# Kernel optimization log

Hardware: AMD Instinct MI355X
Metric: run time of the kernel (lower is better)

## Reference

```python
import jax, jax.numpy as jnp
import numpy as np

B, C, D = 2, 2048, 1024   # batch, seq_len, hidden_size
I = 2048                  # intermediate_size (GLU hidden)
E, K = 8, 2               # n_experts, top_k
CF = 1.25                 # capacity factor


def setup_inputs() -> dict:
    key = jax.random.key(0)
    k1, k2, k3, k4 = jax.random.split(key, 4)
    scale = 0.02
    return {
        "hidden_states": jax.random.normal(k1, (B, C, D), jnp.float32),
        "Wg": jax.random.normal(k2, (E, D), jnp.float32) * scale,      # router gate weight [E, d]
        "W1": jax.random.normal(k3, (E, D, 2 * I), jnp.float32) * scale,  # expert in-proj
        "W2": jax.random.normal(k4, (E, I, D), jnp.float32) * scale,      # expert out-proj
    }


def reference(hidden_states, Wg, W1, W2):
    Bx, Cx, d = hidden_states.shape
    N = Bx * Cx
    cap = int(N * K * CF / E)  # exp_capacity (static)
    x = hidden_states.reshape(N, d)

    # --- router (eval mode: no noise) ---
    logits = x @ Wg.T                          # [N, E]
    top_v, top_i = jax.lax.top_k(logits, K)    # [N, K]
    gates = jax.nn.softmax(top_v, axis=-1)     # [N, K]

    # --- greedy capacity-limited assignment (token-major, then k), vectorized ---
    flat_e = top_i.reshape(N * K)              # expert id per (token, k) slot, in loop order
    gates_f = gates.reshape(N * K)
    tok = jnp.repeat(jnp.arange(N), K)         # token id per slot
    onehot = jax.nn.one_hot(flat_e, E, dtype=jnp.int32)
    pos = jnp.cumsum(onehot, axis=0) - 1       # running count per expert
    pos_f = jnp.take_along_axis(pos, flat_e[:, None], axis=1)[:, 0]
    keep = pos_f < cap                         # slots beyond capacity are dropped
    pos_safe = jnp.where(keep, pos_f, cap)     # out-of-range -> dropped by mode='drop'

    # --- dispatch: exp_batches[e, pos] = x[token] ---
    exp_batches = jnp.zeros((E, cap, d), x.dtype).at[flat_e, pos_safe].set(x[tok], mode='drop')

    # --- per-expert GLU MLP (batched over experts) ---
    h = jnp.einsum('ecd,edf->ecf', exp_batches, W1)       # [E, cap, 2I]
    inp, gate = jnp.split(h, 2, axis=-1)
    h = jax.nn.gelu(inp, approximate=False) * gate        # exact gelu, matches torch
    exp_out = jnp.einsum('eci,eid->ecd', h, W2)           # [E, cap, d]

    # --- combine: equals exp_mask.view(N,-1) @ exp_out.view(-1,d) ---
    gathered = exp_out[flat_e, jnp.minimum(pos_safe, cap - 1)]  # [N*K, d]
    contrib = jnp.where(keep, gates_f, 0.0)[:, None] * gathered
    out = jax.ops.segment_sum(contrib, tok, num_segments=N)    # [N, d]
    return out.reshape(Bx, Cx, d)
```

## Files before the change

### kernel.cpp

```cpp
#include <hip/hip_runtime.h>
#include <hip/hip_bf16.h>
#include <math.h>

#define N_TOK 4096
#define DIM   1024
#define NEXP  8
#define IDIM  2048
#define TWOI  4096
#define CAP   1280

#define W1_BLOCKS (64 * 16 * NEXP)
#define W2_BLOCKS (16 * 32 * NEXP)
#define ROUTER_BLOCKS (N_TOK / 4)

#define G1X 32
#define G1Y 10
#define G1_TRANS_Z ((W2_BLOCKS + G1X * G1Y - 1) / (G1X * G1Y))

using short8  = __attribute__((ext_vector_type(8))) short;
using floatx4 = __attribute__((ext_vector_type(4))) float;

__device__ __forceinline__ unsigned short f2b(float f) {
  __hip_bfloat16 h = __float2bfloat16(f);
  return *reinterpret_cast<unsigned short*>(&h);
}

__device__ __forceinline__ void async16(const unsigned short* g, unsigned short* l) {
  __builtin_amdgcn_global_load_lds(
      (const __attribute__((address_space(1))) unsigned int*)g,
      (__attribute__((address_space(3))) unsigned int*)l,
      16, 0, 0);
}

__global__ __launch_bounds__(256) void prologue_kernel(const float* __restrict__ W1,
                                                       unsigned short* __restrict__ w1t,
                                                       const float* __restrict__ x,
                                                       const float* __restrict__ Wg,
                                                       unsigned short* __restrict__ xb,
                                                       float* __restrict__ out,
                                                       int* __restrict__ top_i,
                                                       float* __restrict__ gates) {
  __shared__ __align__(16) float smem_f[NEXP * DIM];
  int bid = blockIdx.x;
  int tid = threadIdx.x;

  if (bid < W1_BLOCKS) {
    float (*tile)[65] = reinterpret_cast<float (*)[65]>(smem_f);
    int e = bid >> 10;
    int t = bid & 1023;
    const int R = DIM, C = TWOI;
    int r0 = (t & 15) * 64;
    int c0 = (t >> 4) * 64;
    const float* s = W1 + (size_t)e * R * C;
    unsigned short* d = w1t + (size_t)e * R * C;
    int tr = tid >> 4, tc = (tid & 15) * 4;
#pragma unroll
    for (int i = 0; i < 4; i++) {
      float4 v = *reinterpret_cast<const float4*>(&s[(size_t)(r0 + tr + i * 16) * C + c0 + tc]);
      tile[tr + i * 16][tc]     = v.x;
      tile[tr + i * 16][tc + 1] = v.y;
      tile[tr + i * 16][tc + 2] = v.z;
      tile[tr + i * 16][tc + 3] = v.w;
    }
    __syncthreads();
#pragma unroll
    for (int j = 0; j < 4; j++) {
      int c = (tid >> 4) + j * 16;
      int r4 = (tid & 15) * 4;
      ushort4 o;
      o.x = f2b(tile[r4][c]);
      o.y = f2b(tile[r4 + 1][c]);
      o.z = f2b(tile[r4 + 2][c]);
      o.w = f2b(tile[r4 + 3][c]);
      *reinterpret_cast<ushort4*>(&d[(size_t)(c0 + c) * R + r0 + r4]) = o;
    }
  } else {
    int rb = bid - W1_BLOCKS;
    float* wg = smem_f;
    for (int i = tid * 4; i < NEXP * DIM; i += 256 * 4) {
      *reinterpret_cast<float4*>(wg + i) = *reinterpret_cast<const float4*>(Wg + i);
    }
    __syncthreads();
    int wave = tid >> 6, lane = tid & 63;
    int t = rb * 4 + wave;
    const float* xr = x + (size_t)t * DIM;
    unsigned short* xbr = xb + (size_t)t * DIM;
    float* outr = out + (size_t)t * DIM;
    double acc[NEXP];
#pragma unroll
    for (int e = 0; e < NEXP; e++) acc[e] = 0.0;
    for (int i = lane; i < DIM; i += 64) {
      float xf = xr[i];
      xbr[i] = f2b(xf);
      outr[i] = 0.0f;
      double xv = (double)xf;
#pragma unroll
      for (int e = 0; e < NEXP; e++) acc[e] += xv * (double)wg[e * DIM + i];
    }
#pragma unroll
    for (int e = 0; e < NEXP; e++) {
#pragma unroll
      for (int m = 1; m < 64; m <<= 1) acc[e] += __shfl_xor(acc[e], m, 64);
    }
    if (lane == 0) {
      int i0 = 0; double v0 = acc[0];
      for (int e = 1; e < NEXP; e++) { if (acc[e] > v0) { v0 = acc[e]; i0 = e; } }
      int i1 = -1; double v1 = -1e300;
      for (int e = 0; e < NEXP; e++) { if (e != i0 && acc[e] > v1) { v1 = acc[e]; i1 = e; } }
      double e1 = exp(v1 - v0);
      float g0 = (float)(1.0 / (1.0 + e1));
      float g1 = (float)(e1 / (1.0 + e1));
      top_i[t * 2] = i0; top_i[t * 2 + 1] = i1;
      gates[t * 2] = g0; gates[t * 2 + 1] = g1;
    }
  }
}

__global__ __launch_bounds__(1024) void scan_kernel(const int* __restrict__ top_i,
                                                    const float* __restrict__ gates,
                                                    int* __restrict__ rowtok,
                                                    float* __restrict__ rowgate,
                                                    int* __restrict__ cnt) {
  __shared__ int hist[NEXP][1024];
  int t = threadIdx.x;
  int s0 = t * 8;
  int eloc[8];
  int c[NEXP];
#pragma unroll
  for (int e = 0; e < NEXP; e++) c[e] = 0;
#pragma unroll
  for (int j = 0; j < 8; j++) { int e = top_i[s0 + j]; eloc[j] = e; c[e]++; }
#pragma unroll
  for (int e = 0; e < NEXP; e++) hist[e][t] = c[e];
  __syncthreads();
  for (int step = 1; step < 1024; step <<= 1) {
    int tmp[NEXP];
#pragma unroll
    for (int e = 0; e < NEXP; e++) tmp[e] = (t >= step) ? hist[e][t - step] : 0;
    __syncthreads();
#pragma unroll
    for (int e = 0; e < NEXP; e++) hist[e][t] += tmp[e];
    __syncthreads();
  }
  int base[NEXP];
#pragma unroll
  for (int e = 0; e < NEXP; e++) base[e] = hist[e][t] - c[e];
  if (t < NEXP) {
    int tot = hist[t][1023];
    cnt[t] = tot < CAP ? tot : CAP;
  }
#pragma unroll
  for (int j = 0; j < 8; j++) {
    int s = s0 + j;
    int e = eloc[j];
    int pos = base[e]++;
    if (pos < CAP) {
      rowtok[e * CAP + pos] = s >> 1;
      rowgate[e * CAP + pos] = gates[s];
    }
  }
}

__global__ __launch_bounds__(256, 4) void gemm1_kernel(const unsigned short* __restrict__ xb,
                                                       const unsigned short* __restrict__ w1t,
                                                       const int* __restrict__ rowtok,
                                                       const int* __restrict__ cnt,
                                                       unsigned short* __restrict__ H,
                                                       const float* __restrict__ W2,
                                                       unsigned short* __restrict__ w2t) {
  __shared__ __align__(16) unsigned char smem[64 * 65 * 4];
  int tid  = threadIdx.x;
  int z = blockIdx.z;

  if (z >= NEXP) {
    int id = (z - NEXP) * (G1X * G1Y) + blockIdx.y * G1X + blockIdx.x;
    if (id >= W2_BLOCKS) return;
    float (*tile)[65] = reinterpret_cast<float (*)[65]>(smem);
    int e = id >> 9;
    int t = id & 511;
    const int R = IDIM, C = DIM;
    int r0 = (t & 31) * 64;
    int c0 = (t >> 5) * 64;
    const float* s = W2 + (size_t)e * R * C;
    unsigned short* d = w2t + (size_t)e * R * C;
    int tr = tid >> 4, tc = (tid & 15) * 4;
#pragma unroll
    for (int i = 0; i < 4; i++) {
      float4 v = *reinterpret_cast<const float4*>(&s[(size_t)(r0 + tr + i * 16) * C + c0 + tc]);
      tile[tr + i * 16][tc]     = v.x;
      tile[tr + i * 16][tc + 1] = v.y;
      tile[tr + i * 16][tc + 2] = v.z;
      tile[tr + i * 16][tc + 3] = v.w;
    }
    __syncthreads();
#pragma unroll
    for (int j = 0; j < 4; j++) {
      int c = (tid >> 4) + j * 16;
      int r4 = (tid & 15) * 4;
      ushort4 o;
      o.x = f2b(tile[r4][c]);
      o.y = f2b(tile[r4 + 1][c]);
      o.z = f2b(tile[r4 + 2][c]);
      o.w = f2b(tile[r4 + 3][c]);
      *reinterpret_cast<ushort4*>(&d[(size_t)(c0 + c) * R + r0 + r4]) = o;
    }
    return;
  }

  int e  = z;
  int m0 = blockIdx.y * 128;
  int i0 = blockIdx.x * 64;
  int cnte = cnt[e];
  if (m0 >= cnte) return;

  unsigned short* As = reinterpret_cast<unsigned short*>(smem);
  unsigned short* Bi = reinterpret_cast<unsigned short*>(smem + 8192);
  unsigned short* Bg = reinterpret_cast<unsigned short*>(smem + 12288);

  int lane = tid & 63;
  int wave = tid >> 6;

  int srA0 = wave * 32 + (lane >> 2);
  int srA1 = srA0 + 16;
  int srB  = wave * 16 + (lane >> 2);
  int sk   = (lane & 3) * 8;

  int ma0 = m0 + srA0, ma1 = m0 + srA1;
  int tok0 = (ma0 < cnte) ? rowtok[e * CAP + ma0] : 0;
  int tok1 = (ma1 < cnte) ? rowtok[e * CAP + ma1] : 0;

  const unsigned short* w1e = w1t + (size_t)e * TWOI * DIM;
  const unsigned short* gA0 = xb + (size_t)tok0 * DIM + sk;
  const unsigned short* gA1 = xb + (size_t)tok1 * DIM + sk;
  const unsigned short* gBi = w1e + (size_t)(i0 + srB) * DIM + sk;
  const unsigned short* gBg = w1e + (size_t)(i0 + srB + IDIM) * DIM + sk;

  unsigned short* lA0 = As + (wave * 2 + 0) * 512;
  unsigned short* lA1 = As + (wave * 2 + 1) * 512;
  unsigned short* lBi = Bi + wave * 512;
  unsigned short* lBg = Bg + wave * 512;

  int lane16 = lane & 15;
  int quad   = lane >> 4;
  int wm = (wave & 1) * 64;
  int wn = (wave >> 1) * 32;

  floatx4 acc_i[4][2], acc_g[4][2];
#pragma unroll
  for (int i = 0; i < 4; i++)
#pragma unroll
    for (int j = 0; j < 2; j++) {
      acc_i[i][j] = (floatx4){0.f, 0.f, 0.f, 0.f};
      acc_g[i][j] = (floatx4){0.f, 0.f, 0.f, 0.f};
    }

  for (int k0 = 0; k0 < DIM; k0 += 32) {
    __syncthreads();
    async16(gA0 + k0, lA0);
    async16(gA1 + k0, lA1);
    async16(gBi + k0, lBi);
    async16(gBg + k0, lBg);
    __syncthreads();

    short8 a[4];
#pragma unroll
    for (int i = 0; i < 4; i++)
      a[i] = *(const short8*)&As[(wm + i * 16 + lane16) * 32 + quad * 8];
#pragma unroll
    for (int j = 0; j < 2; j++) {
      short8 bi = *(const short8*)&Bi[(wn + j * 16 + lane16) * 32 + quad * 8];
#pragma unroll
      for (int i = 0; i < 4; i++)
        acc_i[i][j] = __builtin_amdgcn_mfma_f32_16x16x32_bf16(a[i], bi, acc_i[i][j], 0, 0, 0);
      short8 bg = *(const short8*)&Bg[(wn + j * 16 + lane16) * 32 + quad * 8];
#pragma unroll
      for (int i = 0; i < 4; i++)
        acc_g[i][j] = __builtin_amdgcn_mfma_f32_16x16x32_bf16(a[i], bg, acc_g[i][j], 0, 0, 0);
    }
  }

  unsigned short* He = H + (size_t)e * CAP * IDIM;
#pragma unroll
  for (int i = 0; i < 4; i++) {
#pragma unroll
    for (int r = 0; r < 4; r++) {
      int m = m0 + wm + i * 16 + quad * 4 + r;
#pragma unroll
      for (int j = 0; j < 2; j++) {
        int n = i0 + wn + j * 16 + lane16;
        float vi = acc_i[i][j][r];
        float vg = acc_g[i][j][r];
        float h = 0.5f * vi * (1.0f + erff(vi * 0.70710678118654752f)) * vg;
        He[(size_t)m * IDIM + n] = f2b(h);
      }
    }
  }
}

__global__ __launch_bounds__(256, 3) void gemm2_kernel(const unsigned short* __restrict__ H,
                                                       const unsigned short* __restrict__ w2t,
                                                       const int* __restrict__ cnt,
                                                       const int* __restrict__ rowtok,
                                                       const float* __restrict__ rowgate,
                                                       float* __restrict__ out) {
  int e  = blockIdx.z & 7;
  int kh = blockIdx.z >> 3;
  int m0 = blockIdx.y * 128;
  int n0 = blockIdx.x * 128;
  int cnte = cnt[e];
  if (m0 >= cnte) return;

  __shared__ __align__(16) unsigned short As[128 * 32];
  __shared__ __align__(16) unsigned short Bs[128 * 32];

  int tid  = threadIdx.x;
  int lane = tid & 63;
  int wave = tid >> 6;

  int sr0 = wave * 32 + (lane >> 2);
  int sr1 = sr0 + 16;
  int sk  = (lane & 3) * 8;
  int kbase = kh * (IDIM / 2);

  const unsigned short* He  = H + (size_t)e * CAP * IDIM;
  const unsigned short* w2e = w2t + (size_t)e * DIM * IDIM;
  const unsigned short* gA0 = He + (size_t)(m0 + sr0) * IDIM + kbase + sk;
  const unsigned short* gA1 = He + (size_t)(m0 + sr1) * IDIM + kbase + sk;
  const unsigned short* gB0 = w2e + (size_t)(n0 + sr0) * IDIM + kbase + sk;
  const unsigned short* gB1 = w2e + (size_t)(n0 + sr1) * IDIM + kbase + sk;

  unsigned short* lA0 = As + (wave * 2 + 0) * 512;
  unsigned short* lA1 = As + (wave * 2 + 1) * 512;
  unsigned short* lB0 = Bs + (wave * 2 + 0) * 512;
  unsigned short* lB1 = Bs + (wave * 2 + 1) * 512;

  int lane16 = lane & 15;
  int quad   = lane >> 4;
  int wm = (wave & 1) * 64;
  int wn = (wave >> 1) * 64;

  floatx4 acc[4][4];
#pragma unroll
  for (int i = 0; i < 4; i++)
#pragma unroll
    for (int j = 0; j < 4; j++) acc[i][j] = (floatx4){0.f, 0.f, 0.f, 0.f};

  for (int k0 = 0; k0 < IDIM / 2; k0 += 32) {
    __syncthreads();
    async16(gA0 + k0, lA0);
    async16(gA1 + k0, lA1);
    async16(gB0 + k0, lB0);
    async16(gB1 + k0, lB1);
    __syncthreads();

    short8 a[4];
#pragma unroll
    for (int i = 0; i < 4; i++)
      a[i] = *(const short8*)&As[(wm + i * 16 + lane16) * 32 + quad * 8];
#pragma unroll
    for (int j = 0; j < 4; j++) {
      short8 b = *(const short8*)&Bs[(wn + j * 16 + lane16) * 32 + quad * 8];
#pragma unroll
      for (int i = 0; i < 4; i++)
        acc[i][j] = __builtin_amdgcn_mfma_f32_16x16x32_bf16(a[i], b, acc[i][j], 0, 0, 0);
    }
  }

#pragma unroll
  for (int i = 0; i < 4; i++) {
#pragma unroll
    for (int r = 0; r < 4; r++) {
      int m = m0 + wm + i * 16 + quad * 4 + r;
      if (m < cnte) {
        int tok = rowtok[e * CAP + m];
        float g = rowgate[e * CAP + m];
        float* orow = out + (size_t)tok * DIM;
#pragma unroll
        for (int j = 0; j < 4; j++) {
          int n = n0 + wn + j * 16 + lane16;
          atomicAdd(orow + n, g * acc[i][j][r]);
        }
      }
    }
  }
}

extern "C" void kernel_launch(void* const* d_in, const int* in_sizes, int n_in,
                              void* d_out, int out_size, void* d_ws, size_t ws_size,
                              hipStream_t stream) {
  const float* x  = (const float*)d_in[0];
  const float* Wg = (const float*)d_in[1];
  const float* W1 = (const float*)d_in[2];
  const float* W2 = (const float*)d_in[3];
  float* out = (float*)d_out;

  char* ws = (char*)d_ws;
  size_t off = 0;
  auto alloc = [&](size_t bytes) -> void* {
    void* p = ws + off;
    off = (off + bytes + 255) & ~(size_t)255;
    return p;
  };
  int*   top_i   = (int*)alloc((size_t)N_TOK * 2 * sizeof(int));
  float* gates   = (float*)alloc((size_t)N_TOK * 2 * sizeof(float));
  int*   rowtok  = (int*)alloc((size_t)NEXP * CAP * sizeof(int));
  float* rowgate = (float*)alloc((size_t)NEXP * CAP * sizeof(float));
  int*   cnt     = (int*)alloc((size_t)NEXP * sizeof(int));
  unsigned short* xb  = (unsigned short*)alloc((size_t)N_TOK * DIM * 2);
  unsigned short* w1t = (unsigned short*)alloc((size_t)NEXP * TWOI * DIM * 2);
  unsigned short* w2t = (unsigned short*)alloc((size_t)NEXP * DIM * IDIM * 2);
  unsigned short* Hb  = (unsigned short*)alloc((size_t)NEXP * CAP * IDIM * 2);
  if (off > ws_size) return;

  hipLaunchKernelGGL(prologue_kernel, dim3(W1_BLOCKS + ROUTER_BLOCKS), dim3(256), 0, stream,
                     W1, w1t, x, Wg, xb, out, top_i, gates);
  hipLaunchKernelGGL(scan_kernel, dim3(1), dim3(1024), 0, stream,
                     top_i, gates, rowtok, rowgate, cnt);
  hipLaunchKernelGGL(gemm1_kernel, dim3(G1X, G1Y, NEXP + G1_TRANS_Z), dim3(256), 0, stream,
                     xb, w1t, rowtok, cnt, Hb, W2, w2t);
  hipLaunchKernelGGL(gemm2_kernel, dim3(DIM / 128, CAP / 128, 16), dim3(256), 0, stream,
                     Hb, w2t, cnt, rowtok, rowgate, out);
}
```

Baseline: 471.5 us.

## Replace gemm2 atomic scatter with partial-sum buffers and a gather combine kernel

gemm2 no longer applies gates and atomically adds into the output. It now writes plain fp32 partial results for each K-half and expert into a workspace buffer. A new combine kernel gathers each token's two expert slots from both halves, applies the gates, and writes the output directly, so the prologue no longer zeroes out. This removes contended float atomics and gives deterministic accumulation, at the cost of an extra ~84MB write plus gather read and one more launch. Gemm2 launch bounds are also raised to target 4 blocks per CU.

```diff
diff --git a/kernel.cpp b/kernel.cpp
--- a/kernel.cpp
+++ b/kernel.cpp
@@ -37,7 +37,6 @@
                                                        const float* __restrict__ x,
                                                        const float* __restrict__ Wg,
                                                        unsigned short* __restrict__ xb,
-                                                       float* __restrict__ out,
                                                        int* __restrict__ top_i,
                                                        float* __restrict__ gates) {
   __shared__ __align__(16) float smem_f[NEXP * DIM];
@@ -85,14 +84,12 @@
     int t = rb * 4 + wave;
     const float* xr = x + (size_t)t * DIM;
     unsigned short* xbr = xb + (size_t)t * DIM;
-    float* outr = out + (size_t)t * DIM;
     double acc[NEXP];
 #pragma unroll
     for (int e = 0; e < NEXP; e++) acc[e] = 0.0;
     for (int i = lane; i < DIM; i += 64) {
       float xf = xr[i];
       xbr[i] = f2b(xf);
-      outr[i] = 0.0f;
       double xv = (double)xf;
 #pragma unroll
       for (int e = 0; e < NEXP; e++) acc[e] += xv * (double)wg[e * DIM + i];
@@ -119,7 +116,8 @@
 __global__ __launch_bounds__(1024) void scan_kernel(const int* __restrict__ top_i,
                                                     const float* __restrict__ gates,
                                                     int* __restrict__ rowtok,
-                                                    float* __restrict__ rowgate,
+                                                    int* __restrict__ slotpos,
+                                                    float* __restrict__ tokgate,
                                                     int* __restrict__ cnt) {
   __shared__ int hist[NEXP][1024];
   int t = threadIdx.x;
@@ -154,10 +152,10 @@
     int s = s0 + j;
     int e = eloc[j];
     int pos = base[e]++;
-    if (pos < CAP) {
-      rowtok[e * CAP + pos] = s >> 1;
-      rowgate[e * CAP + pos] = gates[s];
-    }
+    bool keep = pos < CAP;
+    slotpos[s] = keep ? pos : 0;
+    tokgate[s] = keep ? gates[s] : 0.0f;
+    if (keep) rowtok[e * CAP + pos] = s >> 1;
   }
 }
 
@@ -297,12 +295,10 @@
   }
 }
 
-__global__ __launch_bounds__(256, 3) void gemm2_kernel(const unsigned short* __restrict__ H,
+__global__ __launch_bounds__(256, 4) void gemm2_kernel(const unsigned short* __restrict__ H,
                                                        const unsigned short* __restrict__ w2t,
                                                        const int* __restrict__ cnt,
-                                                       const int* __restrict__ rowtok,
-                                                       const float* __restrict__ rowgate,
-                                                       float* __restrict__ out) {
+                                                       float* __restrict__ expoutP) {
   int e  = blockIdx.z & 7;
   int kh = blockIdx.z >> 3;
   int m0 = blockIdx.y * 128;
@@ -366,23 +362,42 @@
     }
   }
 
+  float* oute = expoutP + ((size_t)kh * NEXP + e) * CAP * DIM;
 #pragma unroll
   for (int i = 0; i < 4; i++) {
 #pragma unroll
     for (int r = 0; r < 4; r++) {
       int m = m0 + wm + i * 16 + quad * 4 + r;
-      if (m < cnte) {
-        int tok = rowtok[e * CAP + m];
-        float g = rowgate[e * CAP + m];
-        float* orow = out + (size_t)tok * DIM;
-#pragma unroll
-        for (int j = 0; j < 4; j++) {
-          int n = n0 + wn + j * 16 + lane16;
-          atomicAdd(orow + n, g * acc[i][j][r]);
-        }
+#pragma unroll
+      for (int j = 0; j < 4; j++) {
+        int n = n0 + wn + j * 16 + lane16;
+        oute[(size_t)m * DIM + n] = acc[i][j][r];
       }
     }
   }
+}
+
+__global__ __launch_bounds__(256) void combine_kernel(const int* __restrict__ top_i,
+                                                      const int* __restrict__ slotpos,
+                                                      const float* __restrict__ tokgate,
+                                                      const float* __restrict__ expoutP,
+                                                      float* __restrict__ out) {
+  int t = blockIdx.x;
+  int tid = threadIdx.x;
+  int e0 = top_i[t * 2], e1 = top_i[t * 2 + 1];
+  int p0 = slotpos[t * 2], p1 = slotpos[t * 2 + 1];
+  float g0 = tokgate[t * 2], g1 = tokgate[t * 2 + 1];
+  const float4* a0 = reinterpret_cast<const float4*>(expoutP + ((size_t)e0 * CAP + p0) * DIM);
+  const float4* a1 = reinterpret_cast<const float4*>(expoutP + ((size_t)(NEXP + e0) * CAP + p0) * DIM);
+  const float4* b0 = reinterpret_cast<const float4*>(expoutP + ((size_t)e1 * CAP + p1) * DIM);
+  const float4* b1 = reinterpret_cast<const float4*>(expoutP + ((size_t)(NEXP + e1) * CAP + p1) * DIM);
+  float4 va0 = a0[tid], va1 = a1[tid], vb0 = b0[tid], vb1 = b1[tid];
+  float4 o;
+  o.x = g0 * (va0.x + va1.x) + g1 * (vb0.x + vb1.x);
+  o.y = g0 * (va0.y + va1.y) + g1 * (vb0.y + vb1.y);
+  o.z = g0 * (va0.z + va1.z) + g1 * (vb0.z + vb1.z);
+  o.w = g0 * (va0.w + va1.w) + g1 * (vb0.w + vb1.w);
+  reinterpret_cast<float4*>(out + (size_t)t * DIM)[tid] = o;
 }
 
 extern "C" void kernel_launch(void* const* d_in, const int* in_sizes, int n_in,
@@ -404,20 +419,24 @@
   int*   top_i   = (int*)alloc((size_t)N_TOK * 2 * sizeof(int));
   float* gates   = (float*)alloc((size_t)N_TOK * 2 * sizeof(float));
   int*   rowtok  = (int*)alloc((size_t)NEXP * CAP * sizeof(int));
-  float* rowgate = (float*)alloc((size_t)NEXP * CAP * sizeof(float));
+  int*   slotpos = (int*)alloc((size_t)N_TOK * 2 * sizeof(int));
+  float* tokgate = (float*)alloc((size_t)N_TOK * 2 * sizeof(float));
   int*   cnt     = (int*)alloc((size_t)NEXP * sizeof(int));
   unsigned short* xb  = (unsigned short*)alloc((size_t)N_TOK * DIM * 2);
   unsigned short* w1t = (unsigned short*)alloc((size_t)NEXP * TWOI * DIM * 2);
   unsigned short* w2t = (unsigned short*)alloc((size_t)NEXP * DIM * IDIM * 2);
   unsigned short* Hb  = (unsigned short*)alloc((size_t)NEXP * CAP * IDIM * 2);
+  float* expoutP = (float*)alloc((size_t)2 * NEXP * CAP * DIM * sizeof(float));
   if (off > ws_size) return;
 
   hipLaunchKernelGGL(prologue_kernel, dim3(W1_BLOCKS + ROUTER_BLOCKS), dim3(256), 0, stream,
-                     W1, w1t, x, Wg, xb, out, top_i, gates);
+                     W1, w1t, x, Wg, xb, top_i, gates);
   hipLaunchKernelGGL(scan_kernel, dim3(1), dim3(1024), 0, stream,
-                     top_i, gates, rowtok, rowgate, cnt);
+                     top_i, gates, rowtok, slotpos, tokgate, cnt);
   hipLaunchKernelGGL(gemm1_kernel, dim3(G1X, G1Y, NEXP + G1_TRANS_Z), dim3(256), 0, stream,
                      xb, w1t, rowtok, cnt, Hb, W2, w2t);
   hipLaunchKernelGGL(gemm2_kernel, dim3(DIM / 128, CAP / 128, 16), dim3(256), 0, stream,
-                     Hb, w2t, cnt, rowtok, rowgate, out);
-}
+                     Hb, w2t, cnt, expoutP);
+  hipLaunchKernelGGL(combine_kernel, dim3(N_TOK), dim3(256), 0, stream,
+                     top_i, slotpos, tokgate, expoutP, out);
+}
```

New measurement: 459.1 us. 1.03x faster.

## Replace atomic combine with per-slot output buffer, drop split-K, double K-step per barrier

Applied to the files above, without the earlier changes.

The second GEMM no longer splits K across two blocks or scatters into the output with atomicAdd. Each (token, slot) row is written once into a scratch buffer, and a new combine kernel sums the two slots per token using the kept-gate mask. Both GEMMs now stage two 32-wide K chunks per barrier pair, halving synchronisations in exchange for more LDS. gemm2 occupancy is raised to 4, and the output-zeroing pass in the prologue is removed. The cost is an extra kernel launch, a 32MB scratch write and read, and fewer gemm2 blocks now that split-K is gone.

```diff
diff --git a/kernel.cpp b/kernel.cpp
--- a/kernel.cpp
+++ b/kernel.cpp
@@ -37,7 +37,6 @@
                                                        const float* __restrict__ x,
                                                        const float* __restrict__ Wg,
                                                        unsigned short* __restrict__ xb,
-                                                       float* __restrict__ out,
                                                        int* __restrict__ top_i,
                                                        float* __restrict__ gates) {
   __shared__ __align__(16) float smem_f[NEXP * DIM];
@@ -85,14 +84,12 @@
     int t = rb * 4 + wave;
     const float* xr = x + (size_t)t * DIM;
     unsigned short* xbr = xb + (size_t)t * DIM;
-    float* outr = out + (size_t)t * DIM;
     double acc[NEXP];
 #pragma unroll
     for (int e = 0; e < NEXP; e++) acc[e] = 0.0;
     for (int i = lane; i < DIM; i += 64) {
       float xf = xr[i];
       xbr[i] = f2b(xf);
-      outr[i] = 0.0f;
       double xv = (double)xf;
 #pragma unroll
       for (int e = 0; e < NEXP; e++) acc[e] += xv * (double)wg[e * DIM + i];
@@ -119,7 +116,9 @@
 __global__ __launch_bounds__(1024) void scan_kernel(const int* __restrict__ top_i,
                                                     const float* __restrict__ gates,
                                                     int* __restrict__ rowtok,
+                                                    int* __restrict__ rowslot,
                                                     float* __restrict__ rowgate,
+                                                    float* __restrict__ tokgate,
                                                     int* __restrict__ cnt) {
   __shared__ int hist[NEXP][1024];
   int t = threadIdx.x;
@@ -154,8 +153,11 @@
     int s = s0 + j;
     int e = eloc[j];
     int pos = base[e]++;
-    if (pos < CAP) {
-      rowtok[e * CAP + pos] = s >> 1;
+    bool keep = pos < CAP;
+    tokgate[s] = keep ? gates[s] : 0.0f;
+    if (keep) {
+      rowtok[e * CAP + pos]  = s >> 1;
+      rowslot[e * CAP + pos] = s & 1;
       rowgate[e * CAP + pos] = gates[s];
     }
   }
@@ -168,7 +170,7 @@
                                                        unsigned short* __restrict__ H,
                                                        const float* __restrict__ W2,
                                                        unsigned short* __restrict__ w2t) {
-  __shared__ __align__(16) unsigned char smem[64 * 65 * 4];
+  __shared__ __align__(16) unsigned char smem[32768];
   int tid  = threadIdx.x;
   int z = blockIdx.z;
 
@@ -213,9 +215,9 @@
   int cnte = cnt[e];
   if (m0 >= cnte) return;
 
-  unsigned short* As = reinterpret_cast<unsigned short*>(smem);
-  unsigned short* Bi = reinterpret_cast<unsigned short*>(smem + 8192);
-  unsigned short* Bg = reinterpret_cast<unsigned short*>(smem + 12288);
+  unsigned short* As[2] = { (unsigned short*)smem,           (unsigned short*)(smem + 8192) };
+  unsigned short* Bi[2] = { (unsigned short*)(smem + 16384), (unsigned short*)(smem + 20480) };
+  unsigned short* Bg[2] = { (unsigned short*)(smem + 24576), (unsigned short*)(smem + 28672) };
 
   int lane = tid & 63;
   int wave = tid >> 6;
@@ -235,11 +237,6 @@
   const unsigned short* gBi = w1e + (size_t)(i0 + srB) * DIM + sk;
   const unsigned short* gBg = w1e + (size_t)(i0 + srB + IDIM) * DIM + sk;
 
-  unsigned short* lA0 = As + (wave * 2 + 0) * 512;
-  unsigned short* lA1 = As + (wave * 2 + 1) * 512;
-  unsigned short* lBi = Bi + wave * 512;
-  unsigned short* lBg = Bg + wave * 512;
-
   int lane16 = lane & 15;
   int quad   = lane >> 4;
   int wm = (wave & 1) * 64;
@@ -254,28 +251,35 @@
       acc_g[i][j] = (floatx4){0.f, 0.f, 0.f, 0.f};
     }
 
-  for (int k0 = 0; k0 < DIM; k0 += 32) {
-    __syncthreads();
-    async16(gA0 + k0, lA0);
-    async16(gA1 + k0, lA1);
-    async16(gBi + k0, lBi);
-    async16(gBg + k0, lBg);
-    __syncthreads();
-
-    short8 a[4];
-#pragma unroll
-    for (int i = 0; i < 4; i++)
-      a[i] = *(const short8*)&As[(wm + i * 16 + lane16) * 32 + quad * 8];
-#pragma unroll
-    for (int j = 0; j < 2; j++) {
-      short8 bi = *(const short8*)&Bi[(wn + j * 16 + lane16) * 32 + quad * 8];
+  for (int k0 = 0; k0 < DIM; k0 += 64) {
+    __syncthreads();
+#pragma unroll
+    for (int b = 0; b < 2; b++) {
+      int kk = k0 + b * 32;
+      async16(gA0 + kk, As[b] + (wave * 2 + 0) * 512);
+      async16(gA1 + kk, As[b] + (wave * 2 + 1) * 512);
+      async16(gBi + kk, Bi[b] + wave * 512);
+      async16(gBg + kk, Bg[b] + wave * 512);
+    }
+    __syncthreads();
+
+#pragma unroll
+    for (int b = 0; b < 2; b++) {
+      short8 a[4];
 #pragma unroll
       for (int i = 0; i < 4; i++)
-        acc_i[i][j] = __builtin_amdgcn_mfma_f32_16x16x32_bf16(a[i], bi, acc_i[i][j], 0, 0, 0);
-      short8 bg = *(const short8*)&Bg[(wn + j * 16 + lane16) * 32 + quad * 8];
-#pragma unroll
-      for (int i = 0; i < 4; i++)
-        acc_g[i][j] = __builtin_amdgcn_mfma_f32_16x16x32_bf16(a[i], bg, acc_g[i][j], 0, 0, 0);
+        a[i] = *(const short8*)&As[b][(wm + i * 16 + lane16) * 32 + quad * 8];
+#pragma unroll
+      for (int j = 0; j < 2; j++) {
+        short8 bi = *(const short8*)&Bi[b][(wn + j * 16 + lane16) * 32 + quad * 8];
+#pragma unroll
+        for (int i = 0; i < 4; i++)
+          acc_i[i][j] = __builtin_amdgcn_mfma_f32_16x16x32_bf16(a[i], bi, acc_i[i][j], 0, 0, 0);
+        short8 bg = *(const short8*)&Bg[b][(wn + j * 16 + lane16) * 32 + quad * 8];
+#pragma unroll
+        for (int i = 0; i < 4; i++)
+          acc_g[i][j] = __builtin_amdgcn_mfma_f32_16x16x32_bf16(a[i], bg, acc_g[i][j], 0, 0, 0);
+      }
     }
   }
 
@@ -297,21 +301,22 @@
   }
 }
 
-__global__ __launch_bounds__(256, 3) void gemm2_kernel(const unsigned short* __restrict__ H,
+__global__ __launch_bounds__(256, 4) void gemm2_kernel(const unsigned short* __restrict__ H,
                                                        const unsigned short* __restrict__ w2t,
                                                        const int* __restrict__ cnt,
                                                        const int* __restrict__ rowtok,
+                                                       const int* __restrict__ rowslot,
                                                        const float* __restrict__ rowgate,
-                                                       float* __restrict__ out) {
-  int e  = blockIdx.z & 7;
-  int kh = blockIdx.z >> 3;
+                                                       float* __restrict__ out2) {
+  int e  = blockIdx.z;
   int m0 = blockIdx.y * 128;
   int n0 = blockIdx.x * 128;
   int cnte = cnt[e];
   if (m0 >= cnte) return;
 
-  __shared__ __align__(16) unsigned short As[128 * 32];
-  __shared__ __align__(16) unsigned short Bs[128 * 32];
+  __shared__ __align__(16) unsigned char smem[32768];
+  unsigned short* As[2] = { (unsigned short*)smem,           (unsigned short*)(smem + 8192) };
+  unsigned short* Bs[2] = { (unsigned short*)(smem + 16384), (unsigned short*)(smem + 24576) };
 
   int tid  = threadIdx.x;
   int lane = tid & 63;
@@ -320,19 +325,13 @@
   int sr0 = wave * 32 + (lane >> 2);
   int sr1 = sr0 + 16;
   int sk  = (lane & 3) * 8;
-  int kbase = kh * (IDIM / 2);
 
   const unsigned short* He  = H + (size_t)e * CAP * IDIM;
   const unsigned short* w2e = w2t + (size_t)e * DIM * IDIM;
-  const unsigned short* gA0 = He + (size_t)(m0 + sr0) * IDIM + kbase + sk;
-  const unsigned short* gA1 = He + (size_t)(m0 + sr1) * IDIM + kbase + sk;
-  const unsigned short* gB0 = w2e + (size_t)(n0 + sr0) * IDIM + kbase + sk;
-  const unsigned short* gB1 = w2e + (size_t)(n0 + sr1) * IDIM + kbase + sk;
-
-  unsigned short* lA0 = As + (wave * 2 + 0) * 512;
-  unsigned short* lA1 = As + (wave * 2 + 1) * 512;
-  unsigned short* lB0 = Bs + (wave * 2 + 0) * 512;
-  unsigned short* lB1 = Bs + (wave * 2 + 1) * 512;
+  const unsigned short* gA0 = He + (size_t)(m0 + sr0) * IDIM + sk;
+  const unsigned short* gA1 = He + (size_t)(m0 + sr1) * IDIM + sk;
+  const unsigned short* gB0 = w2e + (size_t)(n0 + sr0) * IDIM + sk;
+  const unsigned short* gB1 = w2e + (size_t)(n0 + sr1) * IDIM + sk;
 
   int lane16 = lane & 15;
   int quad   = lane >> 4;
@@ -345,24 +344,31 @@
 #pragma unroll
     for (int j = 0; j < 4; j++) acc[i][j] = (floatx4){0.f, 0.f, 0.f, 0.f};
 
-  for (int k0 = 0; k0 < IDIM / 2; k0 += 32) {
-    __syncthreads();
-    async16(gA0 + k0, lA0);
-    async16(gA1 + k0, lA1);
-    async16(gB0 + k0, lB0);
-    async16(gB1 + k0, lB1);
-    __syncthreads();
-
-    short8 a[4];
-#pragma unroll
-    for (int i = 0; i < 4; i++)
-      a[i] = *(const short8*)&As[(wm + i * 16 + lane16) * 32 + quad * 8];
-#pragma unroll
-    for (int j = 0; j < 4; j++) {
-      short8 b = *(const short8*)&Bs[(wn + j * 16 + lane16) * 32 + quad * 8];
+  for (int k0 = 0; k0 < IDIM; k0 += 64) {
+    __syncthreads();
+#pragma unroll
+    for (int b = 0; b < 2; b++) {
+      int kk = k0 + b * 32;
+      async16(gA0 + kk, As[b] + (wave * 2 + 0) * 512);
+      async16(gA1 + kk, As[b] + (wave * 2 + 1) * 512);
+      async16(gB0 + kk, Bs[b] + (wave * 2 + 0) * 512);
+      async16(gB1 + kk, Bs[b] + (wave * 2 + 1) * 512);
+    }
+    __syncthreads();
+
+#pragma unroll
+    for (int b = 0; b < 2; b++) {
+      short8 a[4];
 #pragma unroll
       for (int i = 0; i < 4; i++)
-        acc[i][j] = __builtin_amdgcn_mfma_f32_16x16x32_bf16(a[i], b, acc[i][j], 0, 0, 0);
+        a[i] = *(const short8*)&As[b][(wm + i * 16 + lane16) * 32 + quad * 8];
+#pragma unroll
+      for (int j = 0; j < 4; j++) {
+        short8 bb = *(const short8*)&Bs[b][(wn + j * 16 + lane16) * 32 + quad * 8];
+#pragma unroll
+        for (int i = 0; i < 4; i++)
+          acc[i][j] = __builtin_amdgcn_mfma_f32_16x16x32_bf16(a[i], bb, acc[i][j], 0, 0, 0);
+      }
     }
   }
 
@@ -373,16 +379,34 @@
       int m = m0 + wm + i * 16 + quad * 4 + r;
       if (m < cnte) {
         int tok = rowtok[e * CAP + m];
+        int sl  = rowslot[e * CAP + m];
         float g = rowgate[e * CAP + m];
-        float* orow = out + (size_t)tok * DIM;
+        float* orow = out2 + ((size_t)tok * 2 + sl) * DIM;
 #pragma unroll
         for (int j = 0; j < 4; j++) {
           int n = n0 + wn + j * 16 + lane16;
-          atomicAdd(orow + n, g * acc[i][j][r]);
+          orow[n] = g * acc[i][j][r];
         }
       }
     }
   }
+}
+
+__global__ __launch_bounds__(256) void combine_kernel(const float* __restrict__ tokgate,
+                                                      const float* __restrict__ out2,
+                                                      float* __restrict__ out) {
+  int t = blockIdx.x;
+  int tid = threadIdx.x;
+  float g0 = tokgate[t * 2], g1 = tokgate[t * 2 + 1];
+  const float4* r0 = reinterpret_cast<const float4*>(out2 + (size_t)(t * 2) * DIM);
+  const float4* r1 = reinterpret_cast<const float4*>(out2 + (size_t)(t * 2 + 1) * DIM);
+  float4 a = r0[tid], b = r1[tid];
+  float4 o;
+  o.x = (g0 != 0.0f ? a.x : 0.0f) + (g1 != 0.0f ? b.x : 0.0f);
+  o.y = (g0 != 0.0f ? a.y : 0.0f) + (g1 != 0.0f ? b.y : 0.0f);
+  o.z = (g0 != 0.0f ? a.z : 0.0f) + (g1 != 0.0f ? b.z : 0.0f);
+  o.w = (g0 != 0.0f ? a.w : 0.0f) + (g1 != 0.0f ? b.w : 0.0f);
+  reinterpret_cast<float4*>(out + (size_t)t * DIM)[tid] = o;
 }
 
 extern "C" void kernel_launch(void* const* d_in, const int* in_sizes, int n_in,
@@ -404,20 +428,25 @@
   int*   top_i   = (int*)alloc((size_t)N_TOK * 2 * sizeof(int));
   float* gates   = (float*)alloc((size_t)N_TOK * 2 * sizeof(float));
   int*   rowtok  = (int*)alloc((size_t)NEXP * CAP * sizeof(int));
+  int*   rowslot = (int*)alloc((size_t)NEXP * CAP * sizeof(int));
   float* rowgate = (float*)alloc((size_t)NEXP * CAP * sizeof(float));
+  float* tokgate = (float*)alloc((size_t)N_TOK * 2 * sizeof(float));
   int*   cnt     = (int*)alloc((size_t)NEXP * sizeof(int));
   unsigned short* xb  = (unsigned short*)alloc((size_t)N_TOK * DIM * 2);
   unsigned short* w1t = (unsigned short*)alloc((size_t)NEXP * TWOI * DIM * 2);
   unsigned short* w2t = (unsigned short*)alloc((size_t)NEXP * DIM * IDIM * 2);
   unsigned short* Hb  = (unsigned short*)alloc((size_t)NEXP * CAP * IDIM * 2);
+  float* out2 = (float*)alloc((size_t)N_TOK * 2 * DIM * sizeof(float));
   if (off > ws_size) return;
 
   hipLaunchKernelGGL(prologue_kernel, dim3(W1_BLOCKS + ROUTER_BLOCKS), dim3(256), 0, stream,
-                     W1, w1t, x, Wg, xb, out, top_i, gates);
+                     W1, w1t, x, Wg, xb, top_i, gates);
   hipLaunchKernelGGL(scan_kernel, dim3(1), dim3(1024), 0, stream,
-                     top_i, gates, rowtok, rowgate, cnt);
+                     top_i, gates, rowtok, rowslot, rowgate, tokgate, cnt);
   hipLaunchKernelGGL(gemm1_kernel, dim3(G1X, G1Y, NEXP + G1_TRANS_Z), dim3(256), 0, stream,
                      xb, w1t, rowtok, cnt, Hb, W2, w2t);
-  hipLaunchKernelGGL(gemm2_kernel, dim3(DIM / 128, CAP / 128, 16), dim3(256), 0, stream,
-                     Hb, w2t, cnt, rowtok, rowgate, out);
-}
+  hipLaunchKernelGGL(gemm2_kernel, dim3(DIM / 128, CAP / 128, NEXP), dim3(256), 0, stream,
+                     Hb, w2t, cnt, rowtok, rowslot, rowgate, out2);
+  hipLaunchKernelGGL(combine_kernel, dim3(N_TOK), dim3(256), 0, stream,
+                     tokgate, out2, out);
+}
```

After: 439.4 us. 6.8% less time.
